# Kernel optimization log

Measured on AMD Instinct MI355X. Metric: run time of the kernel, lower is better.

Reference implementation:

```python
import jax, jax.numpy as jnp
import numpy as np

B, X, Y, C = 8, 64, 64, 128       # batch, spatial H, spatial W, n_channels
CTX, N, H, D = 768, 256, 8, 64    # context_dim, context len, n_heads, head_dim
HID = H * D                        # hidden_dim = 512


def _ln(x, w, b):
    # torch nn.LayerNorm: biased variance, eps=1e-5
    mu = x.mean(-1, keepdims=True)
    var = ((x - mu) ** 2).mean(-1, keepdims=True)
    return (x - mu) * jax.lax.rsqrt(var + 1e-5) * w + b


def setup_inputs() -> dict:
    key = jax.random.key(0)
    ks = jax.random.split(key, 8)
    w = lambda k, shape: jax.random.normal(k, shape, jnp.float32) * 0.02
    return {
        "xt": jax.random.normal(ks[0], (B, X, Y, C), jnp.float32),
        "context": jax.random.normal(ks[1], (B, N, CTX), jnp.float32),
        "mask": jax.random.randint(ks[2], (B, N), 0, 2).astype(bool),
        "norm_w": jnp.ones((C,), jnp.float32),
        "norm_b": jnp.zeros((C,), jnp.float32),
        "ctx_norm_w": jnp.ones((CTX,), jnp.float32),
        "ctx_norm_b": jnp.zeros((CTX,), jnp.float32),
        "Wq": w(ks[3], (C, HID)),
        "Wkv": w(ks[4], (CTX, 2 * HID)),
        "null_kv": jax.random.normal(ks[5], (2, D), jnp.float32),
        "Wout": w(ks[6], (HID, C)),
        "bout": jnp.zeros((C,), jnp.float32),
    }


def reference(xt, context, mask, norm_w, norm_b, ctx_norm_w, ctx_norm_b,
              Wq, Wkv, null_kv, Wout, bout):
    xn = _ln(xt, norm_w, norm_b)                     # [B,X,Y,C] (residual uses normed xt, as in source)
    cn = _ln(context, ctx_norm_w, ctx_norm_b)        # [B,N,CTX]

    q = (xn @ Wq).reshape(B, X * Y, H, D).transpose(0, 2, 1, 3)   # b h s d
    k, v = jnp.split(cn @ Wkv, 2, axis=-1)
    k = k.reshape(B, N, H, D).transpose(0, 2, 1, 3)               # b h n d
    v = v.reshape(B, N, H, D).transpose(0, 2, 1, 3)

    nk = jnp.broadcast_to(null_kv[0], (B, H, 1, D))
    nv = jnp.broadcast_to(null_kv[1], (B, H, 1, D))
    k = jnp.concatenate([nk, k], axis=2)                          # b h (n+1) d
    v = jnp.concatenate([nv, v], axis=2)

    scale = D ** -0.5
    sim = jnp.einsum('bhid,bhjd->bhij', q, k) * scale             # [B,H,XY,N+1]
    m = jnp.pad(mask, ((0, 0), (1, 0)), constant_values=True)[:, None, None, :]
    sim = jnp.where(m, sim, -jnp.finfo(sim.dtype).max)

    attn = jax.nn.softmax(sim.astype(jnp.float32), axis=-1)
    out = jnp.einsum('bhij,bhjd->bhid', attn, v)                  # b h s d
    out = out.transpose(0, 2, 1, 3).reshape(B, X, Y, HID)
    return out @ Wout + bout + xn
```

## Files before the change

kernel.cpp:

```cpp
#include <hip/hip_runtime.h>
#include <hip/hip_bf16.h>

typedef unsigned short u16;
typedef unsigned int u32;
typedef __attribute__((ext_vector_type(8))) __bf16 bf16x8;
typedef __attribute__((ext_vector_type(4))) float f32x4;

#define B_    8
#define S_    4096
#define C_    128
#define CTX_  768
#define N_    256
#define H_    8
#define D_    64
#define HID_  512
#define NPAD_ 320

#define QSCALE 0.1803368801111244f

#if __has_builtin(__builtin_amdgcn_exp2f)
#define EXP2(x) __builtin_amdgcn_exp2f(x)
#else
#define EXP2(x) exp2f(x)
#endif

__device__ __forceinline__ float b2f(u16 u) {
    union { u32 i; float f; } v; v.i = ((u32)u) << 16; return v.f;
}
__device__ __forceinline__ u16 f2b(float f) {
    __hip_bfloat16 h = __float2bfloat16(f);
    return *reinterpret_cast<u16*>(&h);
}
__device__ __forceinline__ bool probe_f32(const void* probe) {
    return *(const u32*)probe == 0x3F800000u;
}
__device__ __forceinline__ float ldraw(const void* p_, int i, bool f32m) {
    return f32m ? ((const float*)p_)[i] : b2f(((const u16*)p_)[i]);
}

typedef __attribute__((address_space(1))) const unsigned char gas_char;
typedef __attribute__((address_space(3))) unsigned char las_char;
__device__ __forceinline__ void gld16(const void* g, void* l) {
    __builtin_amdgcn_global_load_lds((gas_char*)g, (las_char*)l, 16, 0, 0);
}

__device__ __forceinline__ void trans64(const void* in, u16* out, int R, int Cc,
                                        int tr, int tc, bool f32m, float scale,
                                        u16 (*tile)[72]) {
    int t = threadIdx.x;
    int r = t >> 2, c4 = (t & 3) * 16;
    size_t ibase = (size_t)(tr * 64 + r) * Cc + tc * 64 + c4;
    if (f32m) {
        const float* fi = (const float*)in;
#pragma unroll
        for (int j = 0; j < 16; ++j) tile[r][c4 + j] = f2b(fi[ibase + j] * scale);
    } else {
        const u16* bi = (const u16*)in;
#pragma unroll
        for (int j = 0; j < 16; ++j) tile[r][c4 + j] = f2b(b2f(bi[ibase + j]) * scale);
    }
    __syncthreads();
    u32 wv[8];
#pragma unroll
    for (int jj = 0; jj < 8; ++jj)
        wv[jj] = (u32)tile[c4 + 2 * jj][r] | ((u32)tile[c4 + 2 * jj + 1][r] << 16);
    u16* orow = out + (size_t)(tc * 64 + r) * R + tr * 64 + c4;
    *(uint4*)orow = *(uint4*)&wv[0];
    *(uint4*)(orow + 8) = *(uint4*)&wv[4];
}

__global__ __launch_bounds__(256) void prep_ln_k(
        const void* nw, const void* nb, const void* cw, const void* cbp,
        const void* nkv, const void* bo, const void* mask_,
        const void* Wq, const void* Wkv, const void* Wout,
        const void* xt, const void* ctx,
        u16* pc, float* mb, u16* WqT, u16* WkvT, u16* WoutT,
        u16* Kat, u16* Vat, u16* xn, u16* cn) {
    __shared__ __align__(16) u16 tile[64][72];
    bool f32m = probe_f32(nw);
    int blk = blockIdx.x, t = threadIdx.x;
    int lane = t & 63, wv = t >> 6;
    if (blk >= 8450) {
        size_t row = (size_t)(blk - 8450) * 4 + wv;
        float f[12]; float s = 0.f, sq = 0.f;
        if (f32m) {
            const float2* px = (const float2*)((const float*)ctx + row * CTX_);
#pragma unroll
            for (int i = 0; i < 6; ++i) {
                float2 v = px[lane + i * 64];
                f[2 * i] = v.x; f[2 * i + 1] = v.y; s += v.x + v.y; sq += v.x * v.x + v.y * v.y;
            }
        } else {
            const u32* px = (const u32*)((const u16*)ctx + row * CTX_);
#pragma unroll
            for (int i = 0; i < 6; ++i) {
                u32 v = px[lane + i * 64];
                float a = b2f((u16)(v & 0xffffu)), c = b2f((u16)(v >> 16));
                f[2 * i] = a; f[2 * i + 1] = c; s += a + c; sq += a * a + c * c;
            }
        }
#pragma unroll
        for (int o = 1; o < 64; o <<= 1) { s += __shfl_xor(s, o); sq += __shfl_xor(sq, o); }
        float mu = s * (1.f / CTX_), var = sq * (1.f / CTX_) - mu * mu;
        float rs = rsqrtf(var + 1e-5f);
        u32* pout = (u32*)(cn + row * CTX_);
#pragma unroll
        for (int i = 0; i < 6; ++i) {
            int col = (lane + i * 64) * 2;
            float o0 = (f[2 * i]     - mu) * rs * ldraw(cw, col, f32m)     + ldraw(cbp, col, f32m);
            float o1 = (f[2 * i + 1] - mu) * rs * ldraw(cw, col + 1, f32m) + ldraw(cbp, col + 1, f32m);
            pout[lane + i * 64] = (u32)f2b(o0) | ((u32)f2b(o1) << 16);
        }
    } else if (blk >= 258) {
        size_t row = (size_t)(blk - 258) * 4 + wv;
        float f0, f1;
        if (f32m) {
            float2 v = ((const float2*)((const float*)xt + row * C_))[lane];
            f0 = v.x; f1 = v.y;
        } else {
            u32 v = ((const u32*)((const u16*)xt + row * C_))[lane];
            f0 = b2f((u16)(v & 0xffffu)); f1 = b2f((u16)(v >> 16));
        }
        float s = f0 + f1, sq = f0 * f0 + f1 * f1;
#pragma unroll
        for (int o = 1; o < 64; o <<= 1) { s += __shfl_xor(s, o); sq += __shfl_xor(sq, o); }
        float mu = s * (1.f / C_);
        float var = sq * (1.f / C_) - mu * mu;
        float rs = rsqrtf(var + 1e-5f);
        float o0 = (f0 - mu) * rs * ldraw(nw, lane * 2, f32m)     + ldraw(nb, lane * 2, f32m);
        float o1 = (f1 - mu) * rs * ldraw(nw, lane * 2 + 1, f32m) + ldraw(nb, lane * 2 + 1, f32m);
        *(u32*)&xn[row * C_ + lane * 2] = (u32)f2b(o0) | ((u32)f2b(o1) << 16);
    } else if (blk < 8) {
        int i = blk * 256 + t;
        const void* src; int off;
        if (i < 128)       { src = nw;  off = i; }
        else if (i < 256)  { src = nb;  off = i - 128; }
        else if (i < 1024) { src = cw;  off = i - 256; }
        else if (i < 1792) { src = cbp; off = i - 1024; }
        else if (i < 1920) { src = nkv; off = i - 1792; }
        else               { src = bo;  off = i - 1920; }
        pc[i] = f2b(ldraw(src, off, f32m));
    } else if (blk < 18) {
        const u32* mu = (const u32*)mask_;
        bool i32m = true;
#pragma unroll
        for (int j = 0; j < 8; ++j) i32m &= (mu[j] <= 1u);
        int i = (blk - 8) * 256 + t;
        if (i < B_ * NPAD_) {
            int b = i / NPAD_, j = i - b * NPAD_;
            bool valid;
            if (j == 0) valid = true;
            else if (j <= N_) valid = i32m ? (((const int*)mask_)[b * N_ + j - 1] != 0)
                                           : (((const unsigned char*)mask_)[b * N_ + j - 1] != 0);
            else valid = false;
            mb[i] = valid ? 0.f : -1e30f;
        }
    } else if (blk < 34) {
        int tb = blk - 18;
        trans64(Wq, WqT, C_, HID_, tb >> 3, tb & 7, f32m, QSCALE, tile);
    } else if (blk < 226) {
        int tb = blk - 34;
        trans64(Wkv, WkvT, CTX_, 2 * HID_, tb >> 4, tb & 15, f32m, 1.f, tile);
    } else if (blk < 242) {
        int tb = blk - 226;
        trans64(Wout, WoutT, HID_, C_, tb >> 1, tb & 1, f32m, 1.f, tile);
    } else {
        int idx = (blk - 242) * 256 + t;
        int d = idx & 63, bh = idx >> 6;
        float kv = ldraw(nkv, d, f32m);
        float vv = ldraw(nkv, 64 + d, f32m);
        Kat[(size_t)bh * NPAD_ * 64 + d] = f2b(kv);
        Vat[((size_t)bh * 64 + d) * NPAD_] = f2b(vv);
        for (int r = 257; r < NPAD_; ++r) {
            Kat[((size_t)bh * NPAD_ + r) * 64 + d] = 0;
            Vat[((size_t)bh * 64 + d) * NPAD_ + r] = 0;
        }
    }
}

template<int EPI, int BM, int BN>
__device__ __forceinline__ void gemm_core(
        u16* As, u16* Bs,
        const u16* __restrict__ A, const u16* __restrict__ Bt,
        int M, int N, int K, int bm, int bn,
        u16* __restrict__ out, u16* __restrict__ out2,
        const u16* __restrict__ resid, const u16* __restrict__ bias, bool f32m) {
    constexpr int MR = BM / 32, NR = BN / 32;
    int tid = threadIdx.x, lane = tid & 63, w = tid >> 6;
    int wr = w >> 1, wc = w & 1;
    int rsel = lane & 15, g = lane >> 4, ksel = g * 8;
    int srow8 = lane >> 3, scol = (lane & 7) * 8;
    const u16* Ab = A + (size_t)(bm * BM) * K;
    const u16* Bb = Bt + (size_t)(bn * BN) * K;
    f32x4 acc[MR][NR] = {};
    for (int k0 = 0; k0 < K; k0 += 64) {
        if (k0) __syncthreads();
#pragma unroll
        for (int i = 0; i < BM / 32; ++i)
            gld16(Ab + (size_t)(i * 32 + w * 8 + srow8) * K + k0 + scol,
                  As + (i * 32 + w * 8) * 64);
#pragma unroll
        for (int i = 0; i < BN / 32; ++i)
            gld16(Bb + (size_t)(i * 32 + w * 8 + srow8) * K + k0 + scol,
                  Bs + (i * 32 + w * 8) * 64);
        __syncthreads();
#pragma unroll
        for (int kk = 0; kk < 2; ++kk) {
            bf16x8 af[MR], bfr[NR];
#pragma unroll
            for (int m = 0; m < MR; ++m)
                af[m] = *(const bf16x8*)&As[(wr * (BM / 2) + m * 16 + rsel) * 64 + kk * 32 + ksel];
#pragma unroll
            for (int n = 0; n < NR; ++n)
                bfr[n] = *(const bf16x8*)&Bs[(wc * (BN / 2) + n * 16 + rsel) * 64 + kk * 32 + ksel];
#pragma unroll
            for (int m = 0; m < MR; ++m)
#pragma unroll
                for (int n = 0; n < NR; ++n)
                    acc[m][n] = __builtin_amdgcn_mfma_f32_16x16x32_bf16(af[m], bfr[n], acc[m][n], 0, 0, 0);
        }
    }
#pragma unroll
    for (int m = 0; m < MR; ++m) {
#pragma unroll
        for (int n = 0; n < NR; ++n) {
            int grow0 = bm * BM + wr * (BM / 2) + m * 16 + g * 4;
            int gcol = bn * BN + wc * (BN / 2) + n * 16 + rsel;
#pragma unroll
            for (int r = 0; r < 4; ++r) {
                int grow = grow0 + r;
                float v = acc[m][n][r];
                if constexpr (EPI == 0) {
                    out[(size_t)grow * N + gcol] = f2b(v);
                } else if constexpr (EPI == 1) {
                    int bb = grow >> 8, nn = grow & 255;
                    if (gcol < 512) {
                        int hh = gcol >> 6, d = gcol & 63;
                        out[((size_t)(bb * 8 + hh) * NPAD_ + nn + 1) * 64 + d] = f2b(v);
                    } else {
                        int hh = (gcol - 512) >> 6, d = gcol & 63;
                        out2[((size_t)(bb * 8 + hh) * 64 + d) * NPAD_ + nn + 1] = f2b(v);
                    }
                } else {
                    float val = v + b2f(resid[(size_t)grow * N + gcol]) + b2f(bias[gcol]);
                    if (f32m) ((float*)out)[(size_t)grow * N + gcol] = val;
                    else out[(size_t)grow * N + gcol] = f2b(val);
                }
            }
        }
    }
}

__global__ __launch_bounds__(256) void qkv_gemm_k(
        const u16* __restrict__ xn, const u16* __restrict__ WqT,
        u16* __restrict__ qbuf,
        const u16* __restrict__ cn, const u16* __restrict__ WkvT,
        u16* __restrict__ Kat, u16* __restrict__ Vat) {
    __shared__ __align__(16) u16 As[128 * 64];
    __shared__ __align__(16) u16 Bs[128 * 64];
    int blk = blockIdx.x;
    if (blk < 1024) {
        gemm_core<0, 128, 128>(As, Bs, xn, WqT, B_ * S_, HID_, C_,
                               blk >> 2, blk & 3, qbuf, nullptr, nullptr, nullptr, false);
    } else {
        int r = blk - 1024;
        gemm_core<1, 64, 64>(As, Bs, cn, WkvT, B_ * N_, 2 * HID_, CTX_,
                             r >> 4, r & 15, Kat, Vat, nullptr, nullptr, false);
    }
}

__global__ __launch_bounds__(256) void out_gemm_k(
        const u16* __restrict__ Obuf, const u16* __restrict__ WoutT,
        u16* __restrict__ out, const u16* __restrict__ xn,
        const u16* __restrict__ bias, const void* probe) {
    __shared__ __align__(16) u16 As[64 * 64];
    __shared__ __align__(16) u16 Bs[64 * 64];
    bool f32m = probe_f32(probe);
    gemm_core<2, 64, 64>(As, Bs, Obuf, WoutT, B_ * S_, C_, HID_,
                         blockIdx.y, blockIdx.x, out, nullptr, xn, bias, f32m);
}

__global__ __launch_bounds__(512) void attn_k(
        const u16* __restrict__ q, const u16* __restrict__ Kat,
        const u16* __restrict__ Vat, const float* __restrict__ mb,
        u16* __restrict__ O) {
    __shared__ __align__(16) u16 Ks[64 * 64];
    __shared__ __align__(16) u16 Vs[64 * 64];
    __shared__ __align__(16) u16 Pl[8][16 * 64];
    __shared__ __align__(16) float Bl[NPAD_];
    int tid = threadIdx.x, lane = tid & 63, w = tid >> 6;
    int qb = blockIdx.x & 31, bh = blockIdx.x >> 5;
    int b = bh >> 3, h = bh & 7;
    int rsel = lane & 15, g = lane >> 4;
    int s0 = qb * 128 + w * 16;
    int swz = (rsel & 7) << 4;

    if (tid < NPAD_) Bl[tid] = mb[b * NPAD_ + tid];

    bf16x8 qf[2];
#pragma unroll
    for (int kk = 0; kk < 2; ++kk)
        qf[kk] = *(const bf16x8*)&q[(size_t)(b * S_ + s0 + rsel) * HID_ + h * 64 + kk * 32 + g * 8];

    const char* Kb = (const char*)(Kat + (size_t)bh * NPAD_ * 64);
    const char* Vb = (const char*)(Vat + (size_t)bh * 64 * NPAD_);
    int srow = w * 8 + (lane >> 3);
    int sbyte = (lane & 7) * 16;
    int swoff = srow * 128 + (sbyte ^ ((srow & 7) << 4));
    u16* PW = &Pl[w][0];

    f32x4 oacc[4] = {};
    float mr = -1e30f, lr = 0.f;

    uint4 kreg = *(const uint4*)(Kb + (size_t)srow * 128 + sbyte);
    uint4 vreg = *(const uint4*)(Vb + (size_t)srow * (NPAD_ * 2) + sbyte);

#pragma unroll
    for (int t = 0; t < 5; ++t) {
        if (t) __syncthreads();
        *(uint4*)((char*)Ks + swoff) = kreg;
        *(uint4*)((char*)Vs + swoff) = vreg;
        __syncthreads();
        if (t < 4) {
            kreg = *(const uint4*)(Kb + (size_t)((t + 1) * 64 + srow) * 128 + sbyte);
            vreg = *(const uint4*)(Vb + (size_t)srow * (NPAD_ * 2) + (t + 1) * 128 + sbyte);
        }

        f32x4 sa[4];
#pragma unroll
        for (int km = 0; km < 4; ++km)
            sa[km] = *(const f32x4*)&Bl[t * 64 + km * 16 + g * 4];
#pragma unroll
        for (int kk = 0; kk < 2; ++kk) {
#pragma unroll
            for (int km = 0; km < 4; ++km) {
                bf16x8 kf = *(const bf16x8*)((const char*)Ks
                        + (km * 16 + rsel) * 128 + ((kk * 64 + g * 16) ^ swz));
                sa[km] = __builtin_amdgcn_mfma_f32_16x16x32_bf16(kf, qf[kk], sa[km], 0, 0, 0);
            }
        }

        float sv[16];
#pragma unroll
        for (int km = 0; km < 4; ++km)
#pragma unroll
            for (int r = 0; r < 4; ++r) sv[km * 4 + r] = sa[km][r];

        float m01 = fmaxf(fmaxf(sv[0], sv[1]), fmaxf(sv[2], sv[3]));
        float m23 = fmaxf(fmaxf(sv[4], sv[5]), fmaxf(sv[6], sv[7]));
        float m45 = fmaxf(fmaxf(sv[8], sv[9]), fmaxf(sv[10], sv[11]));
        float m67 = fmaxf(fmaxf(sv[12], sv[13]), fmaxf(sv[14], sv[15]));
        float tm = fmaxf(fmaxf(m01, m23), fmaxf(m45, m67));
        tm = fmaxf(tm, __shfl_xor(tm, 16));
        tm = fmaxf(tm, __shfl_xor(tm, 32));

        if (!__all(tm <= mr + 8.f)) {
            float mn = fmaxf(mr, tm);
            float corr = EXP2(mr - mn);
            mr = mn;
            lr *= corr;
#pragma unroll
            for (int dm = 0; dm < 4; ++dm)
#pragma unroll
                for (int r = 0; r < 4; ++r) oacc[dm][r] *= corr;
        }

#pragma unroll
        for (int i = 0; i < 16; ++i) sv[i] = EXP2(sv[i] - mr);
        float s01 = (sv[0] + sv[1]) + (sv[2] + sv[3]);
        float s23 = (sv[4] + sv[5]) + (sv[6] + sv[7]);
        float s45 = (sv[8] + sv[9]) + (sv[10] + sv[11]);
        float s67 = (sv[12] + sv[13]) + (sv[14] + sv[15]);
        float ts = (s01 + s23) + (s45 + s67);
        ts += __shfl_xor(ts, 16);
        ts += __shfl_xor(ts, 32);
        lr += ts;

#pragma unroll
        for (int km = 0; km < 4; ++km) {
            uint2 pw;
            pw.x = (u32)f2b(sv[km * 4 + 0]) | ((u32)f2b(sv[km * 4 + 1]) << 16);
            pw.y = (u32)f2b(sv[km * 4 + 2]) | ((u32)f2b(sv[km * 4 + 3]) << 16);
            *(uint2*)((char*)PW + rsel * 128 + ((km * 32 + g * 8) ^ swz)) = pw;
        }

#pragma unroll
        for (int kk = 0; kk < 2; ++kk) {
            bf16x8 pb = *(const bf16x8*)((const char*)PW
                    + rsel * 128 + ((kk * 64 + g * 16) ^ swz));
#pragma unroll
            for (int dm = 0; dm < 4; ++dm) {
                bf16x8 vf = *(const bf16x8*)((const char*)Vs
                        + (dm * 16 + rsel) * 128 + ((kk * 64 + g * 16) ^ swz));
                oacc[dm] = __builtin_amdgcn_mfma_f32_16x16x32_bf16(vf, pb, oacc[dm], 0, 0, 0);
            }
        }
    }

    float inv = 1.f / lr;
#pragma unroll
    for (int dm = 0; dm < 4; ++dm) {
        uint2 pw;
        pw.x = (u32)f2b(oacc[dm][0] * inv) | ((u32)f2b(oacc[dm][1] * inv) << 16);
        pw.y = (u32)f2b(oacc[dm][2] * inv) | ((u32)f2b(oacc[dm][3] * inv) << 16);
        *(uint2*)((char*)PW + rsel * 128 + ((dm * 32 + g * 8) ^ swz)) = pw;
    }
    {
        uint4 r0 = *(const uint4*)((const char*)PW + rsel * 128 + ((g * 16) ^ swz));
        uint4 r1 = *(const uint4*)((const char*)PW + rsel * 128 + (((g + 4) * 16) ^ swz));
        char* dst = (char*)(O + (size_t)(b * S_ + s0 + rsel) * HID_ + h * 64);
        *(uint4*)(dst + g * 16) = r0;
        *(uint4*)(dst + g * 16 + 64) = r1;
    }
}

extern "C" void kernel_launch(void* const* d_in, const int* in_sizes, int n_in,
                              void* d_out, int out_size, void* d_ws, size_t ws_size,
                              hipStream_t stream) {
    const void* xt      = d_in[0];
    const void* context = d_in[1];
    const void* mask    = d_in[2];
    const void* norm_w  = d_in[3];
    const void* norm_b  = d_in[4];
    const void* cnw     = d_in[5];
    const void* cnb     = d_in[6];
    const void* Wq      = d_in[7];
    const void* Wkv     = d_in[8];
    const void* nkv     = d_in[9];
    const void* Wout    = d_in[10];
    const void* bout    = d_in[11];

    char* p = (char*)d_ws;
    u16* pc    = (u16*)p; p += 2048 * 2;
    float* mbf = (float*)p; p += (size_t)B_ * NPAD_ * 4;
    u16* WqT   = (u16*)p; p += (size_t)HID_ * C_ * 2;
    u16* WkvT  = (u16*)p; p += (size_t)2 * HID_ * CTX_ * 2;
    u16* WoutT = (u16*)p; p += (size_t)C_ * HID_ * 2;
    u16* xn    = (u16*)p; p += (size_t)B_ * S_ * C_ * 2;
    u16* cn    = (u16*)p; p += (size_t)B_ * N_ * CTX_ * 2;
    u16* qbuf  = (u16*)p; p += (size_t)B_ * S_ * HID_ * 2;
    u16* Obuf  = (u16*)p; p += (size_t)B_ * S_ * HID_ * 2;
    u16* Kat   = (u16*)p; p += (size_t)B_ * H_ * NPAD_ * 64 * 2;
    u16* Vat   = (u16*)p; p += (size_t)B_ * H_ * 64 * NPAD_ * 2;

    prep_ln_k<<<8962, 256, 0, stream>>>(norm_w, norm_b, cnw, cnb, nkv, bout, mask,
                                        Wq, Wkv, Wout, xt, context,
                                        pc, mbf, WqT, WkvT, WoutT, Kat, Vat, xn, cn);

    qkv_gemm_k<<<1536, 256, 0, stream>>>(xn, WqT, qbuf, cn, WkvT, Kat, Vat);

    attn_k<<<B_ * H_ * (S_ / 128), 512, 0, stream>>>(qbuf, Kat, Vat, mbf, Obuf);

    out_gemm_k<<<dim3(C_ / 64, B_ * S_ / 64), 256, 0, stream>>>(
        Obuf, WoutT, (u16*)d_out, xn, pc + 1920, norm_w);
}
```

Measured before the change: 106.3 us.

## Compact unmasked keys and loop attention only over valid KV tiles

```diff
diff --git a/kernel.cpp b/kernel.cpp
--- a/kernel.cpp
+++ b/kernel.cpp
@@ -74,9 +74,11 @@
         const void* nkv, const void* bo, const void* mask_,
         const void* Wq, const void* Wkv, const void* Wout,
         const void* xt, const void* ctx,
-        u16* pc, float* mb, u16* WqT, u16* WkvT, u16* WoutT,
+        u16* pc, float* mb, int* posmap, int* ntarr,
+        u16* WqT, u16* WkvT, u16* WoutT,
         u16* Kat, u16* Vat, u16* xn, u16* cn) {
     __shared__ __align__(16) u16 tile[64][72];
+    __shared__ int arr[256];
     bool f32m = probe_f32(nw);
     int blk = blockIdx.x, t = threadIdx.x;
     int lane = t & 63, wv = t >> 6;
@@ -140,21 +142,31 @@
         else if (i < 1920) { src = nkv; off = i - 1792; }
         else               { src = bo;  off = i - 1920; }
         pc[i] = f2b(ldraw(src, off, f32m));
-    } else if (blk < 18) {
+    } else if (blk == 8) {
         const u32* mu = (const u32*)mask_;
         bool i32m = true;
 #pragma unroll
         for (int j = 0; j < 8; ++j) i32m &= (mu[j] <= 1u);
-        int i = (blk - 8) * 256 + t;
-        if (i < B_ * NPAD_) {
-            int b = i / NPAD_, j = i - b * NPAD_;
-            bool valid;
-            if (j == 0) valid = true;
-            else if (j <= N_) valid = i32m ? (((const int*)mask_)[b * N_ + j - 1] != 0)
-                                           : (((const unsigned char*)mask_)[b * N_ + j - 1] != 0);
-            else valid = false;
-            mb[i] = valid ? 0.f : -1e30f;
-        }
+        for (int b = 0; b < B_; ++b) {
+            int m = i32m ? (((const int*)mask_)[b * N_ + t] != 0)
+                         : (((const unsigned char*)mask_)[b * N_ + t] != 0);
+            arr[t] = m;
+            __syncthreads();
+            for (int off = 1; off < 256; off <<= 1) {
+                int v = (t >= off) ? arr[t - off] : 0;
+                __syncthreads();
+                arr[t] += v;
+                __syncthreads();
+            }
+            int inclusive = arr[t];
+            int NV = 1 + arr[255];
+            posmap[b * N_ + t] = m ? (1 + inclusive - m) : -1;
+            for (int j = t; j < NPAD_; j += 256)
+                mb[b * NPAD_ + j] = (j < NV) ? 0.f : -1e30f;
+            if (t == 0) ntarr[b] = (NV + 63) >> 6;
+            __syncthreads();
+        }
+    } else if (blk < 18) {
     } else if (blk < 34) {
         int tb = blk - 18;
         trans64(Wq, WqT, C_, HID_, tb >> 3, tb & 7, f32m, QSCALE, tile);
@@ -167,14 +179,8 @@
     } else {
         int idx = (blk - 242) * 256 + t;
         int d = idx & 63, bh = idx >> 6;
-        float kv = ldraw(nkv, d, f32m);
-        float vv = ldraw(nkv, 64 + d, f32m);
-        Kat[(size_t)bh * NPAD_ * 64 + d] = f2b(kv);
-        Vat[((size_t)bh * 64 + d) * NPAD_] = f2b(vv);
-        for (int r = 257; r < NPAD_; ++r) {
-            Kat[((size_t)bh * NPAD_ + r) * 64 + d] = 0;
-            Vat[((size_t)bh * 64 + d) * NPAD_ + r] = 0;
-        }
+        Kat[(size_t)bh * NPAD_ * 64 + d] = f2b(ldraw(nkv, d, f32m));
+        Vat[((size_t)bh * 64 + d) * NPAD_] = f2b(ldraw(nkv, 64 + d, f32m));
     }
 }
 
@@ -184,7 +190,8 @@
         const u16* __restrict__ A, const u16* __restrict__ Bt,
         int M, int N, int K, int bm, int bn,
         u16* __restrict__ out, u16* __restrict__ out2,
-        const u16* __restrict__ resid, const u16* __restrict__ bias, bool f32m) {
+        const u16* __restrict__ resid, const u16* __restrict__ bias,
+        const int* __restrict__ posmap, bool f32m) {
     constexpr int MR = BM / 32, NR = BN / 32;
     int tid = threadIdx.x, lane = tid & 63, w = tid >> 6;
     int wr = w >> 1, wc = w & 1;
@@ -234,12 +241,13 @@
                     out[(size_t)grow * N + gcol] = f2b(v);
                 } else if constexpr (EPI == 1) {
                     int bb = grow >> 8, nn = grow & 255;
-                    if (gcol < 512) {
-                        int hh = gcol >> 6, d = gcol & 63;
-                        out[((size_t)(bb * 8 + hh) * NPAD_ + nn + 1) * 64 + d] = f2b(v);
-                    } else {
-                        int hh = (gcol - 512) >> 6, d = gcol & 63;
-                        out2[((size_t)(bb * 8 + hh) * 64 + d) * NPAD_ + nn + 1] = f2b(v);
+                    int p_ = posmap[bb * N_ + nn];
+                    if (p_ >= 0) {
+                        int hh = (gcol >> 6) & 7, d = gcol & 63;
+                        if (gcol < 512)
+                            out[((size_t)(bb * 8 + hh) * NPAD_ + p_) * 64 + d] = f2b(v);
+                        else
+                            out2[((size_t)(bb * 8 + hh) * 64 + d) * NPAD_ + p_] = f2b(v);
                     }
                 } else {
                     float val = v + b2f(resid[(size_t)grow * N + gcol]) + b2f(bias[gcol]);
@@ -255,17 +263,20 @@
         const u16* __restrict__ xn, const u16* __restrict__ WqT,
         u16* __restrict__ qbuf,
         const u16* __restrict__ cn, const u16* __restrict__ WkvT,
-        u16* __restrict__ Kat, u16* __restrict__ Vat) {
+        u16* __restrict__ Kat, u16* __restrict__ Vat,
+        const int* __restrict__ posmap) {
     __shared__ __align__(16) u16 As[128 * 64];
     __shared__ __align__(16) u16 Bs[128 * 64];
     int blk = blockIdx.x;
     if (blk < 1024) {
         gemm_core<0, 128, 128>(As, Bs, xn, WqT, B_ * S_, HID_, C_,
-                               blk >> 2, blk & 3, qbuf, nullptr, nullptr, nullptr, false);
+                               blk >> 2, blk & 3, qbuf, nullptr, nullptr, nullptr,
+                               nullptr, false);
     } else {
         int r = blk - 1024;
         gemm_core<1, 64, 64>(As, Bs, cn, WkvT, B_ * N_, 2 * HID_, CTX_,
-                             r >> 4, r & 15, Kat, Vat, nullptr, nullptr, false);
+                             r >> 4, r & 15, Kat, Vat, nullptr, nullptr,
+                             posmap, false);
     }
 }
 
@@ -277,13 +288,14 @@
     __shared__ __align__(16) u16 Bs[64 * 64];
     bool f32m = probe_f32(probe);
     gemm_core<2, 64, 64>(As, Bs, Obuf, WoutT, B_ * S_, C_, HID_,
-                         blockIdx.y, blockIdx.x, out, nullptr, xn, bias, f32m);
+                         blockIdx.y, blockIdx.x, out, nullptr, xn, bias,
+                         nullptr, f32m);
 }
 
 __global__ __launch_bounds__(512) void attn_k(
         const u16* __restrict__ q, const u16* __restrict__ Kat,
         const u16* __restrict__ Vat, const float* __restrict__ mb,
-        u16* __restrict__ O) {
+        const int* __restrict__ ntarr, u16* __restrict__ O) {
     __shared__ __align__(16) u16 Ks[64 * 64];
     __shared__ __align__(16) u16 Vs[64 * 64];
     __shared__ __align__(16) u16 Pl[8][16 * 64];
@@ -294,6 +306,7 @@
     int rsel = lane & 15, g = lane >> 4;
     int s0 = qb * 128 + w * 16;
     int swz = (rsel & 7) << 4;
+    int ntb = ntarr[b];
 
     if (tid < NPAD_) Bl[tid] = mb[b * NPAD_ + tid];
 
@@ -315,13 +328,12 @@
     uint4 kreg = *(const uint4*)(Kb + (size_t)srow * 128 + sbyte);
     uint4 vreg = *(const uint4*)(Vb + (size_t)srow * (NPAD_ * 2) + sbyte);
 
-#pragma unroll
-    for (int t = 0; t < 5; ++t) {
+    for (int t = 0; t < ntb; ++t) {
         if (t) __syncthreads();
         *(uint4*)((char*)Ks + swoff) = kreg;
         *(uint4*)((char*)Vs + swoff) = vreg;
         __syncthreads();
-        if (t < 4) {
+        if (t + 1 < ntb) {
             kreg = *(const uint4*)(Kb + (size_t)((t + 1) * 64 + srow) * 128 + sbyte);
             vreg = *(const uint4*)(Vb + (size_t)srow * (NPAD_ * 2) + (t + 1) * 128 + sbyte);
         }
@@ -433,6 +445,8 @@
     char* p = (char*)d_ws;
     u16* pc    = (u16*)p; p += 2048 * 2;
     float* mbf = (float*)p; p += (size_t)B_ * NPAD_ * 4;
+    int* posmap = (int*)p; p += (size_t)B_ * N_ * 4;
+    int* ntarr  = (int*)p; p += 64;
     u16* WqT   = (u16*)p; p += (size_t)HID_ * C_ * 2;
     u16* WkvT  = (u16*)p; p += (size_t)2 * HID_ * CTX_ * 2;
     u16* WoutT = (u16*)p; p += (size_t)C_ * HID_ * 2;
@@ -445,11 +459,12 @@
 
     prep_ln_k<<<8962, 256, 0, stream>>>(norm_w, norm_b, cnw, cnb, nkv, bout, mask,
                                         Wq, Wkv, Wout, xt, context,
-                                        pc, mbf, WqT, WkvT, WoutT, Kat, Vat, xn, cn);
-
-    qkv_gemm_k<<<1536, 256, 0, stream>>>(xn, WqT, qbuf, cn, WkvT, Kat, Vat);
-
-    attn_k<<<B_ * H_ * (S_ / 128), 512, 0, stream>>>(qbuf, Kat, Vat, mbf, Obuf);
+                                        pc, mbf, posmap, ntarr,
+                                        WqT, WkvT, WoutT, Kat, Vat, xn, cn);
+
+    qkv_gemm_k<<<1536, 256, 0, stream>>>(xn, WqT, qbuf, cn, WkvT, Kat, Vat, posmap);
+
+    attn_k<<<B_ * H_ * (S_ / 128), 512, 0, stream>>>(qbuf, Kat, Vat, mbf, ntarr, Obuf);
 
     out_gemm_k<<<dim3(C_ / 64, B_ * S_ / 64), 256, 0, stream>>>(
         Obuf, WoutT, (u16*)d_out, xn, pc + 1920, norm_w);
```

After: 93.25 us. 1.14x faster.
